# Optimization experiments

Hardware: AMD Instinct MI355X
Metric: run time of the kernel (lower is better)

Reference implementation:

```python
import jax, jax.numpy as jnp
import numpy as np

SLICES = [(12, 1), (13, 1)]  # (input_width, hidden_size=1) per slice


def _lstm_last_hidden(xs, W_ih, W_hh, b):
    """Run a standard (PyTorch gate order i,f,g,o) LSTM over time, return last h.
    xs: [T, B, in]; W_ih: [4*H, in]; W_hh: [4*H, H]; b: [4*H] (b_ih + b_hh).
    Returns h_T: [B, H].
    """
    B = xs.shape[1]
    H = W_hh.shape[1]
    h0 = jnp.zeros((B, H), xs.dtype)
    c0 = jnp.zeros((B, H), xs.dtype)

    def step(carry, xt):
        h, c = carry
        gates = xt @ W_ih.T + h @ W_hh.T + b  # [B, 4H]
        i, f, g, o = jnp.split(gates, 4, axis=-1)
        i = jax.nn.sigmoid(i)
        f = jax.nn.sigmoid(f)
        g = jnp.tanh(g)
        o = jax.nn.sigmoid(o)
        c = f * c + i * g
        h = o * jnp.tanh(c)
        return (h, c), None

    (hT, _), _ = jax.lax.scan(step, (h0, c0), xs)
    return hT


def setup_inputs() -> dict:
    key = jax.random.key(0)
    ks = jax.random.split(key, 9)
    B, T, F = 4096, 512, 25
    nb_out = 1
    s = 0.1
    x = jax.random.normal(ks[0], (B, T, F), dtype=jnp.float32)
    # slice-1 LSTM (input 12, hidden 1)
    W_ih1 = jax.random.normal(ks[1], (4, 12), dtype=jnp.float32) * s
    W_hh1 = jax.random.normal(ks[2], (4, 1), dtype=jnp.float32) * s
    b1 = jax.random.normal(ks[3], (4,), dtype=jnp.float32) * s
    # slice-2 LSTM (input 13, hidden 1)
    W_ih2 = jax.random.normal(ks[4], (4, 13), dtype=jnp.float32) * s
    W_hh2 = jax.random.normal(ks[5], (4, 1), dtype=jnp.float32) * s
    b2 = jax.random.normal(ks[6], (4,), dtype=jnp.float32) * s
    # output head Linear(2, nb_out)
    W_out = jax.random.normal(ks[7], (nb_out, 2), dtype=jnp.float32) * s
    b_out = jax.random.normal(ks[8], (nb_out,), dtype=jnp.float32) * s
    return {"x": x, "W_ih1": W_ih1, "W_hh1": W_hh1, "b1": b1,
            "W_ih2": W_ih2, "W_hh2": W_hh2, "b2": b2,
            "W_out": W_out, "b_out": b_out}


def reference(x, W_ih1, W_hh1, b1, W_ih2, W_hh2, b2, W_out, b_out):
    # x: [B, T, 25] -> time-major [T, B, 25]
    xs = jnp.transpose(x, (1, 0, 2))
    h1 = _lstm_last_hidden(xs[..., :12], W_ih1, W_hh1, b1)   # [B, 1]
    h2 = _lstm_last_hidden(xs[..., 12:], W_ih2, W_hh2, b2)   # [B, 1]
    h = jnp.concatenate([h1, h2], axis=-1)                   # [B, 2] == lstm_out[:, -1, :]
    out = h @ W_out.T + b_out                                # [B, nb_out]
    return jax.nn.sigmoid(out)
```

## Files before the change

### kernel.cpp

```cpp
#include <hip/hip_runtime.h>
#include <hip/hip_fp16.h>
#include <stdint.h>


#define T_STEPS 512
#define F_IN    25
#define CH      8
#define LOG2E   1.44269504088896340736f
#define SC1     (-LOG2E)
#define SC2     (-2.0f * LOG2E)

__global__ void __launch_bounds__(256, 2)
k1_gates(const float* __restrict__ x,
         const float* __restrict__ Wih1, const float* __restrict__ b1,
         const float* __restrict__ Wih2, const float* __restrict__ b2,
         uint4* __restrict__ z, int B)
{
  const int tid = threadIdx.x;
  const int c   = tid & 7;
  const int tl  = tid >> 3;
  const int b   = blockIdx.x * CH + c;

  float w1[48], w2[52], bb[8];
#pragma unroll
  for (int j = 0; j < 4; ++j) {
    const float s = (j == 2) ? SC2 : SC1;
#pragma unroll
    for (int f = 0; f < 12; ++f) w1[j * 12 + f] = Wih1[j * 12 + f] * s;
#pragma unroll
    for (int f = 0; f < 13; ++f) w2[j * 13 + f] = Wih2[j * 13 + f] * s;
    bb[j]     = b1[j] * s;
    bb[4 + j] = b2[j] * s;
  }

  const float* __restrict__ xrow = x + (size_t)b * (T_STEPS * F_IN);

  for (int k = 0; k < T_STEPS / 32; ++k) {
    const int t = k * 32 + tl;
    const float* __restrict__ xr = xrow + t * F_IN;

    float xv[25];
#pragma unroll
    for (int f = 0; f < 25; ++f) xv[f] = xr[f];

    float zz[8];
#pragma unroll
    for (int j = 0; j < 8; ++j) zz[j] = bb[j];
#pragma unroll
    for (int f = 0; f < 12; ++f) {
#pragma unroll
      for (int j = 0; j < 4; ++j) zz[j] = fmaf(w1[j * 12 + f], xv[f], zz[j]);
    }
#pragma unroll
    for (int f = 0; f < 13; ++f) {
#pragma unroll
      for (int j = 0; j < 4; ++j) zz[4 + j] = fmaf(w2[j * 13 + f], xv[12 + f], zz[4 + j]);
    }

    const __half2 p0 = __floats2half2_rn(zz[0], zz[1]);
    const __half2 p1 = __floats2half2_rn(zz[2], zz[3]);
    const __half2 p2 = __floats2half2_rn(zz[4], zz[5]);
    const __half2 p3 = __floats2half2_rn(zz[6], zz[7]);
    uint4 q;
    q.x = *(const unsigned int*)&p0;
    q.y = *(const unsigned int*)&p1;
    q.z = *(const unsigned int*)&p2;
    q.w = *(const unsigned int*)&p3;
    z[(size_t)t * B + b] = q;
  }
}

__device__ __forceinline__ void lstm_step(const uint2 v,
                                          const float wi, const float wf,
                                          const float wg, const float wo,
                                          float& h, float& cc) {
  const __half2 h01 = *(const __half2*)&v.x;
  const __half2 h23 = *(const __half2*)&v.y;
  const float2 f01 = __half22float2(h01);
  const float2 f23 = __half22float2(h23);
  const float ei = __builtin_amdgcn_exp2f(fmaf(h, wi, f01.x));
  const float ef = __builtin_amdgcn_exp2f(fmaf(h, wf, f01.y));
  const float eg = __builtin_amdgcn_exp2f(fmaf(h, wg, f23.x));
  const float eo = __builtin_amdgcn_exp2f(fmaf(h, wo, f23.y));
  const float af  = __builtin_amdgcn_rcpf(1.0f + ef);
  const float rig = __builtin_amdgcn_rcpf((1.0f + ei) * (1.0f + eg));
  const float ig  = (1.0f - eg) * rig;
  cc = fmaf(af, cc, ig);
  const float ec  = __builtin_amdgcn_exp2f(cc * SC2);
  const float roc = __builtin_amdgcn_rcpf((1.0f + eo) * (1.0f + ec));
  h = (1.0f - ec) * roc;
}

__global__ void __launch_bounds__(64, 1)
k2_scan(const uint2* __restrict__ z,
        const float* __restrict__ Whh1, const float* __restrict__ Whh2,
        const float* __restrict__ Wout, const float* __restrict__ bout,
        float* __restrict__ out, int B)
{
  const int l    = threadIdx.x;
  const int bb   = blockIdx.x * 32 + (l >> 1);
  const int lstm = l & 1;

  const float* wp = lstm ? Whh2 : Whh1;
  const float wi = SC1 * wp[0];
  const float wf = SC1 * wp[1];
  const float wg = SC2 * wp[2];
  const float wo = SC1 * wp[3];

  const uint2* __restrict__ zp = z + (size_t)bb * 2 + lstm;
  const size_t stride = (size_t)B * 2;

  uint2 rb[8];
#pragma unroll
  for (int j = 0; j < 8; ++j) rb[j] = zp[(size_t)j * stride];

  float h = 0.0f, cc = 0.0f;

  for (int t0 = 0; t0 < T_STEPS - 8; t0 += 8) {
#pragma unroll
    for (int j = 0; j < 8; ++j) {
      const uint2 v = rb[j];
      rb[j] = zp[(size_t)(t0 + j + 8) * stride];
      lstm_step(v, wi, wf, wg, wo, h, cc);
    }
  }
#pragma unroll
  for (int j = 0; j < 8; ++j) lstm_step(rb[j], wi, wf, wg, wo, h, cc);

  const float hp = __shfl_xor(h, 1);
  if (lstm == 0) {
    const float p = fmaf(Wout[0], h, fmaf(Wout[1], hp, bout[0]));
    out[bb] = __builtin_amdgcn_rcpf(1.0f + __builtin_amdgcn_exp2f(p * SC1));
  }
}

extern "C" void kernel_launch(void* const* d_in, const int* in_sizes, int n_in,
                              void* d_out, int out_size, void* d_ws, size_t ws_size,
                              hipStream_t stream) {
  const float* x    = (const float*)d_in[0];
  const float* Wih1 = (const float*)d_in[1];
  const float* Whh1 = (const float*)d_in[2];
  const float* b1   = (const float*)d_in[3];
  const float* Wih2 = (const float*)d_in[4];
  const float* Whh2 = (const float*)d_in[5];
  const float* b2   = (const float*)d_in[6];
  const float* Wout = (const float*)d_in[7];
  const float* bout = (const float*)d_in[8];
  float* out = (float*)d_out;

  const int B = in_sizes[0] / (T_STEPS * F_IN);

  hipLaunchKernelGGL(k1_gates, dim3(B / CH), dim3(256), 0, stream,
                     x, Wih1, b1, Wih2, b2, (uint4*)d_ws, B);
  hipLaunchKernelGGL(k2_scan, dim3(B / 32), dim3(64), 0, stream,
                     (const uint2*)d_ws, Whh1, Whh2, Wout, bout, out, B);
}
```

Baseline: 344.6 us.

## Stage x tiles through double-buffered LDS with coalesced float4 prefetch in gates kernel

```diff
diff --git a/kernel.cpp b/kernel.cpp
--- a/kernel.cpp
+++ b/kernel.cpp
@@ -6,6 +6,12 @@
 #define T_STEPS 512
 #define F_IN    25
 #define CH      8
+#define TC      32
+#define NT      (T_STEPS / TC)
+#define ROWF    (TC * F_IN)
+#define XPAD    8
+#define XROW    (ROWF + XPAD)
+#define TILE4   (CH * ROWF / 4)
 #define LOG2E   1.44269504088896340736f
 #define SC1     (-LOG2E)
 #define SC2     (-2.0f * LOG2E)
@@ -16,10 +22,13 @@
          const float* __restrict__ Wih2, const float* __restrict__ b2,
          uint4* __restrict__ z, int B)
 {
+  __shared__ __align__(16) float xs[2][CH * XROW];
+
   const int tid = threadIdx.x;
   const int c   = tid & 7;
   const int tl  = tid >> 3;
-  const int b   = blockIdx.x * CH + c;
+  const int b0  = blockIdx.x * CH;
+  const int b   = b0 + c;
 
   float w1[48], w2[52], bb[8];
 #pragma unroll
@@ -33,30 +42,54 @@
     bb[4 + j] = b2[j] * s;
   }
 
-  const float* __restrict__ xrow = x + (size_t)b * (T_STEPS * F_IN);
+  const float* gsrc[7];
+  int   ldst[7];
+  bool  act[7];
+#pragma unroll
+  for (int r = 0; r < 7; ++r) {
+    const int j = tid + 256 * r;
+    act[r] = (j < TILE4);
+    const int lc   = j / (ROWF / 4);
+    const int loff = j - lc * (ROWF / 4);
+    gsrc[r] = x + (size_t)(b0 + (act[r] ? lc : 0)) * (T_STEPS * F_IN) + loff * 4;
+    ldst[r] = lc * XROW + loff * 4;
+  }
 
-  for (int k = 0; k < T_STEPS / 32; ++k) {
-    const int t = k * 32 + tl;
-    const float* __restrict__ xr = xrow + t * F_IN;
+  float4 stg[7];
+#pragma unroll
+  for (int r = 0; r < 7; ++r)
+    if (act[r]) stg[r] = *(const float4*)(gsrc[r]);
+#pragma unroll
+  for (int r = 0; r < 7; ++r)
+    if (act[r]) *(float4*)(&xs[0][ldst[r]]) = stg[r];
+#pragma unroll
+  for (int r = 0; r < 7; ++r)
+    if (act[r]) stg[r] = *(const float4*)(gsrc[r] + ROWF);
 
-    float xv[25];
+  for (int k = 0; k < NT; ++k) {
+    __syncthreads();
+    if (k + 1 < NT) {
 #pragma unroll
-    for (int f = 0; f < 25; ++f) xv[f] = xr[f];
+      for (int r = 0; r < 7; ++r)
+        if (act[r]) *(float4*)(&xs[(k + 1) & 1][ldst[r]]) = stg[r];
+    }
 
+    const float* __restrict__ xr = &xs[k & 1][c * XROW + tl * F_IN];
     float zz[8];
 #pragma unroll
     for (int j = 0; j < 8; ++j) zz[j] = bb[j];
 #pragma unroll
     for (int f = 0; f < 12; ++f) {
+      const float xv = xr[f];
 #pragma unroll
-      for (int j = 0; j < 4; ++j) zz[j] = fmaf(w1[j * 12 + f], xv[f], zz[j]);
+      for (int j = 0; j < 4; ++j) zz[j] = fmaf(w1[j * 12 + f], xv, zz[j]);
     }
 #pragma unroll
     for (int f = 0; f < 13; ++f) {
+      const float xv = xr[12 + f];
 #pragma unroll
-      for (int j = 0; j < 4; ++j) zz[4 + j] = fmaf(w2[j * 13 + f], xv[12 + f], zz[4 + j]);
+      for (int j = 0; j < 4; ++j) zz[4 + j] = fmaf(w2[j * 13 + f], xv, zz[4 + j]);
     }
-
     const __half2 p0 = __floats2half2_rn(zz[0], zz[1]);
     const __half2 p1 = __floats2half2_rn(zz[2], zz[3]);
     const __half2 p2 = __floats2half2_rn(zz[4], zz[5]);
@@ -66,7 +99,13 @@
     q.y = *(const unsigned int*)&p1;
     q.z = *(const unsigned int*)&p2;
     q.w = *(const unsigned int*)&p3;
-    z[(size_t)t * B + b] = q;
+    z[(size_t)(k * TC + tl) * B + b] = q;
+
+    if (k + 2 < NT) {
+#pragma unroll
+      for (int r = 0; r < 7; ++r)
+        if (act[r]) stg[r] = *(const float4*)(gsrc[r] + (size_t)(k + 2) * ROWF);
+    }
   }
 }
 
```

Result: slower. 422.4 us (+22.6%).

## Stage x tiles into LDS via async global_load_lds triple buffering

Applied to the files above, without the earlier changes.

```diff
diff --git a/kernel.cpp b/kernel.cpp
--- a/kernel.cpp
+++ b/kernel.cpp
@@ -5,21 +5,34 @@
 
 #define T_STEPS 512
 #define F_IN    25
-#define CH      8
+#define TC      32
+#define NT      (T_STEPS / TC)
+#define CPW     2
+#define ROWF    (TC * F_IN)
+#define TILEF   (CPW * ROWF)
+#define TILE4   (TILEF / 4)
 #define LOG2E   1.44269504088896340736f
 #define SC1     (-LOG2E)
 #define SC2     (-2.0f * LOG2E)
 
-__global__ void __launch_bounds__(256, 2)
+typedef const __attribute__((address_space(1))) void* as1_cvp;
+typedef __attribute__((address_space(3)))       void* as3_vp;
+
+__device__ __forceinline__ void gll16(const float* gsrc, const float* ldst) {
+  __builtin_amdgcn_global_load_lds((as1_cvp)(uintptr_t)gsrc,
+                                   (as3_vp)(uint32_t)(uintptr_t)ldst, 16, 0, 0);
+}
+
+__global__ void __launch_bounds__(64)
 k1_gates(const float* __restrict__ x,
          const float* __restrict__ Wih1, const float* __restrict__ b1,
          const float* __restrict__ Wih2, const float* __restrict__ b2,
          uint4* __restrict__ z, int B)
 {
-  const int tid = threadIdx.x;
-  const int c   = tid & 7;
-  const int tl  = tid >> 3;
-  const int b   = blockIdx.x * CH + c;
+  __shared__ __align__(16) float xs[3 * TILEF];
+
+  const int l  = threadIdx.x;
+  const int b0 = blockIdx.x * CPW;
 
   float w1[48], w2[52], bb[8];
 #pragma unroll
@@ -33,30 +46,55 @@
     bb[4 + j] = b2[j] * s;
   }
 
-  const float* __restrict__ xrow = x + (size_t)b * (T_STEPS * F_IN);
+  const float* gp[7];
+  bool act[7];
+#pragma unroll
+  for (int r = 0; r < 7; ++r) {
+    const int q = l + 64 * r;
+    act[r] = (q < TILE4);
+    const int chain = (q < 200) ? 0 : 1;
+    const int off4  = q - chain * 200;
+    gp[r] = x + (size_t)(b0 + chain) * (T_STEPS * F_IN) + (size_t)off4 * 4;
+  }
 
-  for (int k = 0; k < T_STEPS / 32; ++k) {
-    const int t = k * 32 + tl;
-    const float* __restrict__ xr = xrow + t * F_IN;
+  #define STAGE(tile, bufidx)                                            \
+    {                                                                    \
+      const float* lb = xs + (bufidx) * TILEF;                           \
+      _Pragma("unroll")                                                  \
+      for (int r = 0; r < 7; ++r)                                        \
+        if (act[r]) gll16(gp[r] + (size_t)(tile) * ROWF, lb + r * 256);  \
+    }
 
-    float xv[25];
+  const int c  = l >> 5;
+  const int tl = l & 31;
+  const int b  = b0 + c;
+
+  STAGE(0, 0)
+  STAGE(1, 1)
+
 #pragma unroll
-    for (int f = 0; f < 25; ++f) xv[f] = xr[f];
+  for (int k = 0; k < NT; ++k) {
+    const int tn = (k + 2 < NT) ? (k + 2) : (NT - 1);
+    STAGE(tn, (k + 2) % 3)
 
+    asm volatile("s_waitcnt vmcnt(14)" ::: "memory");
+
+    const float* __restrict__ xr = xs + (k % 3) * TILEF + c * ROWF + tl * F_IN;
     float zz[8];
 #pragma unroll
     for (int j = 0; j < 8; ++j) zz[j] = bb[j];
 #pragma unroll
     for (int f = 0; f < 12; ++f) {
+      const float xv = xr[f];
 #pragma unroll
-      for (int j = 0; j < 4; ++j) zz[j] = fmaf(w1[j * 12 + f], xv[f], zz[j]);
+      for (int j = 0; j < 4; ++j) zz[j] = fmaf(w1[j * 12 + f], xv, zz[j]);
     }
 #pragma unroll
     for (int f = 0; f < 13; ++f) {
+      const float xv = xr[12 + f];
 #pragma unroll
-      for (int j = 0; j < 4; ++j) zz[4 + j] = fmaf(w2[j * 13 + f], xv[12 + f], zz[4 + j]);
+      for (int j = 0; j < 4; ++j) zz[4 + j] = fmaf(w2[j * 13 + f], xv, zz[4 + j]);
     }
-
     const __half2 p0 = __floats2half2_rn(zz[0], zz[1]);
     const __half2 p1 = __floats2half2_rn(zz[2], zz[3]);
     const __half2 p2 = __floats2half2_rn(zz[4], zz[5]);
@@ -66,8 +104,9 @@
     q.y = *(const unsigned int*)&p1;
     q.z = *(const unsigned int*)&p2;
     q.w = *(const unsigned int*)&p3;
-    z[(size_t)t * B + b] = q;
+    z[(size_t)(k * TC + tl) * B + b] = q;
   }
+  #undef STAGE
 }
 
 __device__ __forceinline__ void lstm_step(const uint2 v,
@@ -91,7 +130,7 @@
   h = (1.0f - ec) * roc;
 }
 
-__global__ void __launch_bounds__(64, 1)
+__global__ void __launch_bounds__(64)
 k2_scan(const uint2* __restrict__ z,
         const float* __restrict__ Whh1, const float* __restrict__ Whh2,
         const float* __restrict__ Wout, const float* __restrict__ bout,
@@ -110,22 +149,22 @@
   const uint2* __restrict__ zp = z + (size_t)bb * 2 + lstm;
   const size_t stride = (size_t)B * 2;
 
-  uint2 rb[8];
+  uint2 rb[16];
 #pragma unroll
-  for (int j = 0; j < 8; ++j) rb[j] = zp[(size_t)j * stride];
+  for (int j = 0; j < 16; ++j) rb[j] = zp[(size_t)j * stride];
 
   float h = 0.0f, cc = 0.0f;
 
-  for (int t0 = 0; t0 < T_STEPS - 8; t0 += 8) {
+  for (int t0 = 0; t0 < T_STEPS - 16; t0 += 16) {
 #pragma unroll
-    for (int j = 0; j < 8; ++j) {
+    for (int j = 0; j < 16; ++j) {
       const uint2 v = rb[j];
-      rb[j] = zp[(size_t)(t0 + j + 8) * stride];
+      rb[j] = zp[(size_t)(t0 + j + 16) * stride];
       lstm_step(v, wi, wf, wg, wo, h, cc);
     }
   }
 #pragma unroll
-  for (int j = 0; j < 8; ++j) lstm_step(rb[j], wi, wf, wg, wo, h, cc);
+  for (int j = 0; j < 16; ++j) lstm_step(rb[j], wi, wf, wg, wo, h, cc);
 
   const float hp = __shfl_xor(h, 1);
   if (lstm == 0) {
@@ -150,7 +189,7 @@
 
   const int B = in_sizes[0] / (T_STEPS * F_IN);
 
-  hipLaunchKernelGGL(k1_gates, dim3(B / CH), dim3(256), 0, stream,
+  hipLaunchKernelGGL(k1_gates, dim3(B / CPW), dim3(64), 0, stream,
                      x, Wih1, b1, Wih2, b2, (uint4*)d_ws, B);
   hipLaunchKernelGGL(k2_scan, dim3(B / 32), dim3(64), 0, stream,
                      (const uint2*)d_ws, Whh1, Whh2, Wout, bout, out, B);
```

Measured after the change: 361.4 us. 4.9% more time.
